# Performance work log

Hardware: AMD Instinct MI355X
Metric: run time of the kernel (lower is better)

## Reference

```python
import jax, jax.numpy as jnp
import numpy as np

EPS = 1e-7
ATTN_W_EPS = float(np.sqrt(EPS))
RESIDUAL_SCALE = 1.0


def mish(v):
    return v * jnp.tanh(jax.nn.softplus(v))


def setup_inputs() -> dict:
    key = jax.random.key(0)
    ks = jax.random.split(key, 12)
    N, E, dim, hidden = 100000, 500000, 128, 128
    x = jax.random.normal(ks[0], (N, dim), dtype=jnp.float32)
    edge_attr = jax.random.normal(ks[1], (E, dim), dtype=jnp.float32)
    head_node_index = jax.random.randint(ks[2], (E,), 0, N)
    tail_node_index = jax.random.randint(ks[3], (E,), 0, N)
    node_batch = jax.random.randint(ks[4], (N,), 0, 8)
    edge_batch = jax.random.randint(ks[5], (E,), 0, 8)
    s_in = 1.0 / np.sqrt(dim)
    s_out = 1.0 / np.sqrt(hidden)
    W_node_in = jax.random.normal(ks[6], (dim, 4 * hidden), dtype=jnp.float32) * s_in
    W_edge_in = jax.random.normal(ks[7], (dim, 3 * hidden), dtype=jnp.float32) * s_in
    node_message_bias = jnp.zeros((hidden,), dtype=jnp.float32)
    edge_message_bias = jnp.zeros((hidden,), dtype=jnp.float32)
    W_node_out = jax.random.normal(ks[8], (hidden, dim), dtype=jnp.float32) * s_out
    b_node_out = jnp.zeros((dim,), dtype=jnp.float32)
    W_edge_out = jax.random.normal(ks[9], (hidden, dim), dtype=jnp.float32) * s_out
    b_edge_out = jnp.zeros((dim,), dtype=jnp.float32)
    return {
        'x': x, 'edge_attr': edge_attr,
        'head_node_index': head_node_index, 'tail_node_index': tail_node_index,
        'node_batch': node_batch, 'edge_batch': edge_batch,
        'num_nodes': N, 'num_graphs': 8,
        'W_node_in': W_node_in, 'W_edge_in': W_edge_in,
        'node_message_bias': node_message_bias, 'edge_message_bias': edge_message_bias,
        'W_node_out': W_node_out, 'b_node_out': b_node_out,
        'W_edge_out': W_edge_out, 'b_edge_out': b_edge_out,
    }


def reference(x, edge_attr, head_node_index, tail_node_index, node_batch, edge_batch,
              num_nodes, num_graphs, W_node_in, W_edge_in,
              node_message_bias, edge_message_bias,
              W_node_out, b_node_out, W_edge_out, b_edge_out):
    hidden = node_message_bias.shape[0]
    # node input linear -> 4 chunks
    node_messages = x @ W_node_in  # [N, 4*hidden]
    node_to_self, node_to_neighbor, head_to_edge, tail_to_edge = jnp.split(node_messages, 4, axis=-1)
    node_to_edge = head_to_edge[head_node_index] + tail_to_edge[tail_node_index]  # [E, hidden]
    # edge input linear -> 3 chunks
    edge_messages = edge_attr @ W_edge_in  # [E, 3*hidden]
    edge_to_self, edge_to_tail, edge_attn_message = jnp.split(edge_messages, 3, axis=-1)
    # segment-softmax-style attention weight (max detached, per tail node)
    seg_max = jax.ops.segment_max(jax.lax.stop_gradient(edge_attn_message), tail_node_index,
                                  num_segments=num_nodes)  # [N, hidden]
    edge_attn_weight = jnp.exp(edge_attn_message - seg_max[tail_node_index]) + ATTN_W_EPS  # [E, hidden]
    # attention-weighted scatter aggregation to tail nodes
    sent = (node_to_neighbor[head_node_index] + edge_to_tail) * edge_attn_weight  # [E, hidden]
    received = jax.ops.segment_sum(sent, tail_node_index, num_segments=num_nodes)
    recv_weight = jax.ops.segment_sum(edge_attn_weight, tail_node_index, num_segments=num_nodes)
    node_received = received / (recv_weight + EPS)  # [N, hidden]
    # node output path
    x_residual = mish(node_received + node_to_self + node_message_bias) @ W_node_out + b_node_out
    x_out = x + RESIDUAL_SCALE * x_residual
    # edge output path
    e_residual = mish(node_to_edge + edge_to_self + edge_message_bias) @ W_edge_out + b_edge_out
    edge_attr_out = edge_attr + RESIDUAL_SCALE * e_residual
    return (x_out, edge_attr_out)
```

## Files before the change

kernel.cpp:

```cpp
#include <hip/hip_runtime.h>
#include <hip/hip_bf16.h>
#include <math.h>

typedef short bf16x8 __attribute__((ext_vector_type(8)));
typedef float f32x4 __attribute__((ext_vector_type(4)));
typedef unsigned int u32;
typedef unsigned short u16;

#define DIM 128
#define ATTN_EPS 3.1622776601683794e-4f
#define DIV_EPS 1e-7f
#define SCAN_BLKS 256

__device__ __forceinline__ u16 f2b(float f) {
  u32 u = __float_as_uint(f);
  return (u16)((u + 0x7FFFu + ((u >> 16) & 1u)) >> 16);
}
__device__ __forceinline__ float b2f(u16 s) { return __uint_as_float(((u32)s) << 16); }
__device__ __forceinline__ float mish_f(float v) {
  float e = __expf(fminf(v, 15.f));
  float w = 1.f + e;
  return v * (1.f - 2.f * __builtin_amdgcn_rcpf(w * w + 1.f));
}

template <int NT, int NR>
__device__ __forceinline__ void stage_f32(u16 (*dst)[136], const float* __restrict__ src,
                                          long rowbase, long nrows, int tid) {
  #pragma unroll
  for (int it = 0; it < NR * 16 / NT; ++it) {
    int i = it * NT + tid;
    int r = i >> 4, c = (i & 15) * 8;
    long gr = rowbase + r;
    bf16x8 v;
    if (gr < nrows) {
      const f32x4* p = (const f32x4*)(src + gr * (long)DIM + c);
      f32x4 a = p[0], b = p[1];
      #pragma unroll
      for (int j = 0; j < 4; ++j) { v[j] = (short)f2b(a[j]); v[j + 4] = (short)f2b(b[j]); }
    } else {
      #pragma unroll
      for (int j = 0; j < 8; ++j) v[j] = 0;
    }
    *(bf16x8*)&dst[r][c] = v;
  }
}

template <int NT, int NR>
__device__ __forceinline__ void stage_b16(u16 (*dst)[136], const u16* __restrict__ src, int tid) {
  #pragma unroll
  for (int it = 0; it < NR * 16 / NT; ++it) {
    int i = it * NT + tid;
    int r = i >> 4, c = (i & 15) * 8;
    *(bf16x8*)&dst[r][c] = *(const bf16x8*)&src[(long)r * DIM + c];
  }
}

template <int NT, int NR>
__device__ __forceinline__ void gather_nm(u16 (*dst)[136], const u16* __restrict__ nm,
    const int* __restrict__ idx, int segoff, long rowbase, long nrows, int tid) {
  #pragma unroll
  for (int it = 0; it < NR * 16 / NT; ++it) {
    int i = it * NT + tid;
    int r = i >> 4, c = (i & 15) * 8;
    long gr = rowbase + r;
    bf16x8 v;
    if (gr < nrows) {
      v = *(const bf16x8*)&nm[(long)idx[gr] * 512 + segoff + c];
    } else {
      #pragma unroll
      for (int j = 0; j < 8; ++j) v[j] = 0;
    }
    *(bf16x8*)&dst[r][c] = v;
  }
}

__device__ __forceinline__ void mm_32x64(const u16 (*As)[136], const u16 (*Bs)[136],
                                         int wr, int wc, int lane, f32x4 acc[2][4]) {
  int r0 = wr * 32 + (lane & 15);
  int cb = wc * 64 + (lane & 15);
  int koff = (lane >> 4) * 8;
  #pragma unroll
  for (int ks = 0; ks < 4; ++ks) {
    int k = ks * 32 + koff;
    bf16x8 a0 = *(const bf16x8*)&As[r0][k];
    bf16x8 a1 = *(const bf16x8*)&As[r0 + 16][k];
    #pragma unroll
    for (int ct = 0; ct < 4; ++ct) {
      bf16x8 b = *(const bf16x8*)&Bs[cb + ct * 16][k];
      acc[0][ct] = __builtin_amdgcn_mfma_f32_16x16x32_bf16(a0, b, acc[0][ct], 0, 0, 0);
      acc[1][ct] = __builtin_amdgcn_mfma_f32_16x16x32_bf16(a1, b, acc[1][ct], 0, 0, 0);
    }
  }
}

__global__ void k_prep(const float* __restrict__ Wni, const float* __restrict__ Wei,
                       const float* __restrict__ Wno, const float* __restrict__ Weo,
                       u16* __restrict__ Tni, u16* __restrict__ Tei,
                       u16* __restrict__ Tno, u16* __restrict__ Teo,
                       u32* __restrict__ deg, int N) {
  int stride = gridDim.x * blockDim.x;
  int t0 = blockIdx.x * blockDim.x + threadIdx.x;
  for (int i = t0; i < 128 * 512; i += stride) { int k = i >> 9, c = i & 511; Tni[c * 128 + k] = f2b(Wni[i]); }
  for (int i = t0; i < 128 * 384; i += stride) { int k = i / 384, c = i % 384; Tei[c * 128 + k] = f2b(Wei[i]); }
  for (int i = t0; i < 128 * 128; i += stride) { int k = i >> 7, c = i & 127; Tno[c * 128 + k] = f2b(Wno[i]); }
  for (int i = t0; i < 128 * 128; i += stride) { int k = i >> 7, c = i & 127; Teo[c * 128 + k] = f2b(Weo[i]); }
  for (int i = t0; i < N; i += stride) deg[i] = 0;
}

__global__ __launch_bounds__(512, 4) void k_node_in(const float* __restrict__ x,
    const u16* __restrict__ Tni, u16* __restrict__ nm, int N) {
  __shared__ u16 As[128][136];
  __shared__ u16 Bs[128][136];
  int tid = threadIdx.x, lane = tid & 63;
  int wid = tid >> 6, wr = wid >> 1, wc = wid & 1;
  long rowbase = (long)blockIdx.x * 128;
  stage_f32<512, 128>(As, x, rowbase, N, tid);
  stage_b16<512, 128>(Bs, Tni, tid);
  __syncthreads();
  #pragma unroll 1
  for (int chunk = 0; chunk < 4; ++chunk) {
    f32x4 acc[2][4] = {};
    mm_32x64(As, Bs, wr, wc, lane, acc);
    __syncthreads();
    if (chunk < 3) stage_b16<512, 128>(Bs, Tni + (chunk + 1) * 128 * DIM, tid);
    #pragma unroll
    for (int rt = 0; rt < 2; ++rt)
    #pragma unroll
    for (int j = 0; j < 4; ++j) {
      int lr = wr * 32 + rt * 16 + ((lane >> 4) << 2) + j;
      long r = rowbase + lr;
      if (r >= N) continue;
      #pragma unroll
      for (int ct = 0; ct < 4; ++ct) {
        int col = wc * 64 + ct * 16 + (lane & 15);
        nm[r * 512 + chunk * 128 + col] = f2b(acc[rt][ct][j]);
      }
    }
    if (chunk < 3) __syncthreads();
  }
}

__global__ __launch_bounds__(512, 4) void k_edge_in(const float* __restrict__ ea,
    const u16* __restrict__ Tei, const u16* __restrict__ Teo,
    const u16* __restrict__ nm, const int* __restrict__ head, const int* __restrict__ tail,
    const float* __restrict__ ebias, const float* __restrict__ beo,
    u32* __restrict__ em, float* __restrict__ eout, int E) {
  __shared__ u16 As[128][136];
  __shared__ u16 Bs[128][136];
  int tid = threadIdx.x, lane = tid & 63;
  int wid = tid >> 6, wr = wid >> 1, wc = wid & 1;
  long rowbase = (long)blockIdx.x * 128;
  int col0 = wc * 64 + (lane & 15);

  stage_f32<512, 128>(As, ea, rowbase, E, tid);
  stage_b16<512, 128>(Bs, Tei + 128 * DIM, tid);
  __syncthreads();
  f32x4 acc_t[2][4] = {};
  mm_32x64(As, Bs, wr, wc, lane, acc_t);
  __syncthreads();
  stage_b16<512, 128>(Bs, Tei + 256 * DIM, tid);
  __syncthreads();
  f32x4 acc_m[2][4] = {};
  mm_32x64(As, Bs, wr, wc, lane, acc_m);
  __syncthreads();
  gather_nm<512, 128>(Bs, nm, head, 128, rowbase, E, tid);
  __syncthreads();
  #pragma unroll
  for (int rt = 0; rt < 2; ++rt)
  #pragma unroll
  for (int j = 0; j < 4; ++j) {
    int lr = wr * 32 + rt * 16 + ((lane >> 4) << 2) + j;
    long r = rowbase + lr;
    if (r < E) {
      #pragma unroll
      for (int ct = 0; ct < 4; ++ct) {
        int col = col0 + ct * 16;
        float n2n = b2f(Bs[lr][col]);
        em[r * 128 + col] = (u32)f2b(n2n + acc_t[rt][ct][j])
                          | ((u32)f2b(acc_m[rt][ct][j]) << 16);
      }
    }
  }
  __syncthreads();
  stage_b16<512, 128>(Bs, Tei, tid);
  __syncthreads();
  f32x4 acc_s[2][4] = {};
  mm_32x64(As, Bs, wr, wc, lane, acc_s);
  __syncthreads();
  gather_nm<512, 128>(Bs, nm, head, 256, rowbase, E, tid);
  gather_nm<512, 128>(As, nm, tail, 384, rowbase, E, tid);
  __syncthreads();
  #pragma unroll
  for (int rt = 0; rt < 2; ++rt)
  #pragma unroll
  for (int j = 0; j < 4; ++j) {
    int lr = wr * 32 + rt * 16 + ((lane >> 4) << 2) + j;
    long r = rowbase + lr;
    #pragma unroll
    for (int ct = 0; ct < 4; ++ct) {
      int col = col0 + ct * 16;
      if (r < E) {
        float epre = acc_s[rt][ct][j] + b2f(Bs[lr][col]) + b2f(As[lr][col]) + ebias[col];
        As[lr][col] = f2b(mish_f(epre));
      } else {
        As[lr][col] = 0;
      }
    }
  }
  __syncthreads();
  stage_b16<512, 128>(Bs, Teo, tid);
  __syncthreads();
  f32x4 acc_o[2][4] = {};
  mm_32x64(As, Bs, wr, wc, lane, acc_o);
  #pragma unroll
  for (int rt = 0; rt < 2; ++rt)
  #pragma unroll
  for (int j = 0; j < 4; ++j) {
    int lr = wr * 32 + rt * 16 + ((lane >> 4) << 2) + j;
    long r = rowbase + lr;
    if (r >= E) continue;
    #pragma unroll
    for (int ct = 0; ct < 4; ++ct) {
      int col = col0 + ct * 16;
      eout[r * DIM + col] = ea[r * DIM + col] + acc_o[rt][ct][j] + beo[col];
    }
  }
}

__global__ void k_count(const int* __restrict__ tail, u32* __restrict__ deg, int E) {
  int i = blockIdx.x * blockDim.x + threadIdx.x;
  int stride = gridDim.x * blockDim.x;
  for (; i < E; i += stride) atomicAdd(&deg[tail[i]], 1u);
}
__global__ __launch_bounds__(256) void k_scan_part(const u32* __restrict__ deg,
                                                   u32* __restrict__ part, int N) {
  __shared__ u32 red[256];
  int tid = threadIdx.x, b = blockIdx.x;
  int chunk = (N + SCAN_BLKS - 1) / SCAN_BLKS;
  int lo = b * chunk, hi = min(lo + chunk, N);
  u32 s = 0;
  for (int i = lo + tid; i < hi; i += 256) s += deg[i];
  red[tid] = s; __syncthreads();
  for (int st = 128; st > 0; st >>= 1) { if (tid < st) red[tid] += red[tid + st]; __syncthreads(); }
  if (tid == 0) part[b] = red[0];
}
__global__ __launch_bounds__(256) void k_scan_mid(u32* __restrict__ part) {
  __shared__ u32 lds[256];
  int tid = threadIdx.x;
  u32 v = part[tid];
  lds[tid] = v; __syncthreads();
  for (int s = 1; s < 256; s <<= 1) {
    u32 a = (tid >= s) ? lds[tid - s] : 0; __syncthreads();
    lds[tid] += a; __syncthreads();
  }
  part[tid] = lds[tid] - v;
}
__global__ __launch_bounds__(256) void k_scan_fin(const u32* __restrict__ deg,
    const u32* __restrict__ part, u32* __restrict__ off, u32* __restrict__ cur, int N) {
  __shared__ u32 lds[256];
  int tid = threadIdx.x, b = blockIdx.x;
  int chunk = (N + SCAN_BLKS - 1) / SCAN_BLKS;
  int lo = b * chunk, hi = min(lo + chunk, N);
  u32 carry = part[b];
  for (int base = lo; base < hi; base += 256) {
    int i = base + tid;
    u32 v = (i < hi) ? deg[i] : 0;
    lds[tid] = v; __syncthreads();
    for (int s = 1; s < 256; s <<= 1) {
      u32 a = (tid >= s) ? lds[tid - s] : 0; __syncthreads();
      lds[tid] += a; __syncthreads();
    }
    u32 incl = lds[tid], total = lds[255];
    __syncthreads();
    if (i < hi) { u32 o = carry + incl - v; off[i] = o; cur[i] = o; }
    carry += total;
  }
}
__global__ void k_fill(const int* __restrict__ tail, u32* __restrict__ cur,
                       u32* __restrict__ csr, int E) {
  int i = blockIdx.x * blockDim.x + threadIdx.x;
  int stride = gridDim.x * blockDim.x;
  for (; i < E; i += stride) { u32 p = atomicAdd(&cur[tail[i]], 1u); csr[p] = (u32)i; }
}

__global__ __launch_bounds__(256, 8) void k_node_agg(const u32* __restrict__ em,
    const u16* __restrict__ nm, const u32* __restrict__ off, const u32* __restrict__ deg,
    const u32* __restrict__ csr, const float* __restrict__ nbias,
    u16* __restrict__ hbuf, int N) {
  int tid = threadIdx.x, lane = tid & 63;
  int node = blockIdx.x * 4 + (tid >> 6);
  if (node >= N) return;
  int ch = lane * 2;
  u32 o = __builtin_amdgcn_readfirstlane(off[node]);
  u32 d = __builtin_amdgcn_readfirstlane(deg[node]);
  float m0 = -INFINITY, m1 = -INFINITY;
  float s0 = 0.f, s1 = 0.f, v0 = 0.f, v1 = 0.f, sv0 = 0.f, sv1 = 0.f;
  for (u32 i = 0; i < d; i += 4) {
    uint2 b[4];
    #pragma unroll
    for (int j = 0; j < 4; ++j) {
      if (i + j < d) {
        u32 e = csr[o + i + j];
        b[j] = *(const uint2*)(em + (long)e * 128 + ch);
      } else {
        b[j].x = 0xFF800000u; b[j].y = 0xFF800000u;
      }
    }
    #pragma unroll
    for (int j = 0; j < 4; ++j) {
      float val0 = b2f((u16)(b[j].x & 0xffff)), g0 = b2f((u16)(b[j].x >> 16));
      float val1 = b2f((u16)(b[j].y & 0xffff)), g1 = b2f((u16)(b[j].y >> 16));
      float nmx0 = fmaxf(m0, g0);
      float sc0 = __expf(m0 - nmx0), pe0 = __expf(g0 - nmx0);
      s0 = s0 * sc0 + pe0; v0 = v0 * sc0 + pe0 * val0; sv0 += val0; m0 = nmx0;
      float nmx1 = fmaxf(m1, g1);
      float sc1 = __expf(m1 - nmx1), pe1 = __expf(g1 - nmx1);
      s1 = s1 * sc1 + pe1; v1 = v1 * sc1 + pe1 * val1; sv1 += val1; m1 = nmx1;
    }
  }
  float de = (float)d * ATTN_EPS;
  float r0 = (v0 + ATTN_EPS * sv0) * __builtin_amdgcn_rcpf(s0 + de + DIV_EPS);
  float r1 = (v1 + ATTN_EPS * sv1) * __builtin_amdgcn_rcpf(s1 + de + DIV_EPS);
  u32 np = *(const u32*)&nm[(long)node * 512 + ch];
  float h0 = mish_f(r0 + b2f((u16)(np & 0xffff)) + nbias[ch]);
  float h1 = mish_f(r1 + b2f((u16)(np >> 16)) + nbias[ch + 1]);
  *(u32*)&hbuf[(long)node * 128 + ch] = (u32)f2b(h0) | ((u32)f2b(h1) << 16);
}

__global__ __launch_bounds__(256) void k_node_out(const float* __restrict__ x,
    const u16* __restrict__ hbuf, const u16* __restrict__ Tno, const float* __restrict__ bno,
    float* __restrict__ xout, int N) {
  __shared__ u16 As[64][136];
  __shared__ u16 Bs[128][136];
  int tid = threadIdx.x, lane = tid & 63;
  int wid = tid >> 6, wr = wid >> 1, wc = wid & 1;
  long rowbase = (long)blockIdx.x * 64;
  stage_b16<256, 64>(As, hbuf + rowbase * DIM, tid);
  stage_b16<256, 128>(Bs, Tno, tid);
  __syncthreads();
  f32x4 acc[2][4] = {};
  mm_32x64(As, Bs, wr, wc, lane, acc);
  #pragma unroll
  for (int rt = 0; rt < 2; ++rt)
  #pragma unroll
  for (int j = 0; j < 4; ++j) {
    int lr = wr * 32 + rt * 16 + ((lane >> 4) << 2) + j;
    long r = rowbase + lr;
    if (r >= N) continue;
    #pragma unroll
    for (int ct = 0; ct < 4; ++ct) {
      int col = wc * 64 + ct * 16 + (lane & 15);
      xout[r * DIM + col] = x[r * DIM + col] + acc[rt][ct][j] + bno[col];
    }
  }
}

extern "C" void kernel_launch(void* const* d_in, const int* in_sizes, int n_in,
                              void* d_out, int out_size, void* d_ws, size_t ws_size,
                              hipStream_t stream) {
  const float* x     = (const float*)d_in[0];
  const float* ea    = (const float*)d_in[1];
  const int*   head  = (const int*)d_in[2];
  const int*   tail  = (const int*)d_in[3];
  const float* Wni   = (const float*)d_in[8];
  const float* Wei   = (const float*)d_in[9];
  const float* nbias = (const float*)d_in[10];
  const float* ebias = (const float*)d_in[11];
  const float* Wno   = (const float*)d_in[12];
  const float* bno   = (const float*)d_in[13];
  const float* Weo   = (const float*)d_in[14];
  const float* beo   = (const float*)d_in[15];
  const int N = in_sizes[0] / DIM;
  const int E = in_sizes[1] / DIM;
  const int NB64 = (N + 63) / 64;
  const int NB128 = (N + 127) / 128;
  const int EB = (E + 127) / 128;
  const int NPAD = NB64 * 64;

  char* ws = (char*)d_ws;
  u16*   nm   = (u16*)ws; ws += (size_t)N * 512 * 2;
  u32*   em   = (u32*)ws; ws += (size_t)E * 128 * 4;
  u16*   hbuf = (u16*)ws; ws += (size_t)NPAD * 128 * 2;
  u32*   deg  = (u32*)ws; ws += (size_t)N * 4;
  u32*   off  = (u32*)ws; ws += (size_t)N * 4;
  u32*   cur  = (u32*)ws; ws += (size_t)N * 4;
  u32*   part = (u32*)ws; ws += (size_t)SCAN_BLKS * 4;
  u32*   csr  = (u32*)ws; ws += (size_t)E * 4;
  u16* Tni = (u16*)ws; ws += 512 * DIM * 2;
  u16* Tei = (u16*)ws; ws += 384 * DIM * 2;
  u16* Tno = (u16*)ws; ws += DIM * DIM * 2;
  u16* Teo = (u16*)ws; ws += DIM * DIM * 2;

  float* xout = (float*)d_out;
  float* eout = xout + (size_t)N * DIM;

  k_prep<<<256, 256, 0, stream>>>(Wni, Wei, Wno, Weo, Tni, Tei, Tno, Teo, deg, N);
  k_count<<<512, 256, 0, stream>>>(tail, deg, E);
  k_scan_part<<<SCAN_BLKS, 256, 0, stream>>>(deg, part, N);
  k_scan_mid<<<1, 256, 0, stream>>>(part);
  k_scan_fin<<<SCAN_BLKS, 256, 0, stream>>>(deg, part, off, cur, N);
  k_fill<<<512, 256, 0, stream>>>(tail, cur, csr, E);
  k_node_in<<<NB128, 512, 0, stream>>>(x, Tni, nm, N);
  k_edge_in<<<EB, 512, 0, stream>>>(ea, Tei, Teo, nm, head, tail, ebias, beo, em, eout, E);
  k_node_agg<<<(N + 3) / 4, 256, 0, stream>>>(em, nm, off, deg, csr, nbias, hbuf, N);
  k_node_out<<<NB64, 256, 0, stream>>>(x, hbuf, Tno, bno, xout, N);
}
```

Before: 557.2 us.

## Fuse node aggregation with node output GEMM via LDS-staged hidden tile

Merges the attention aggregation kernel and the node output matmul into a single kernel. Each 512-thread block aggregates 64 nodes (8 per wave), writes the mish-activated hidden rows into shared memory, then runs the 64x128 output GEMM directly from LDS. This removes the hbuf round trip through global memory and one kernel launch. The trade-offs are a serial loop of 8 nodes per wave, which reduces latency hiding on the irregular gathers, and extra LDS per block, which may lower occupancy.

```diff
diff --git a/kernel.cpp b/kernel.cpp
--- a/kernel.cpp
+++ b/kernel.cpp
@@ -86,6 +86,25 @@
     bf16x8 a1 = *(const bf16x8*)&As[r0 + 16][k];
     #pragma unroll
     for (int ct = 0; ct < 4; ++ct) {
+      bf16x8 b = *(const bf16x8*)&Bs[cb + ct * 16][k];
+      acc[0][ct] = __builtin_amdgcn_mfma_f32_16x16x32_bf16(a0, b, acc[0][ct], 0, 0, 0);
+      acc[1][ct] = __builtin_amdgcn_mfma_f32_16x16x32_bf16(a1, b, acc[1][ct], 0, 0, 0);
+    }
+  }
+}
+
+__device__ __forceinline__ void mm_32x32(const u16 (*As)[136], const u16 (*Bs)[136],
+                                         int wr, int wc, int lane, f32x4 acc[2][2]) {
+  int r0 = wr * 32 + (lane & 15);
+  int cb = wc * 32 + (lane & 15);
+  int koff = (lane >> 4) * 8;
+  #pragma unroll
+  for (int ks = 0; ks < 4; ++ks) {
+    int k = ks * 32 + koff;
+    bf16x8 a0 = *(const bf16x8*)&As[r0][k];
+    bf16x8 a1 = *(const bf16x8*)&As[r0 + 16][k];
+    #pragma unroll
+    for (int ct = 0; ct < 2; ++ct) {
       bf16x8 b = *(const bf16x8*)&Bs[cb + ct * 16][k];
       acc[0][ct] = __builtin_amdgcn_mfma_f32_16x16x32_bf16(a0, b, acc[0][ct], 0, 0, 0);
       acc[1][ct] = __builtin_amdgcn_mfma_f32_16x16x32_bf16(a1, b, acc[1][ct], 0, 0, 0);
@@ -283,63 +302,65 @@
   for (; i < E; i += stride) { u32 p = atomicAdd(&cur[tail[i]], 1u); csr[p] = (u32)i; }
 }
 
-__global__ __launch_bounds__(256, 8) void k_node_agg(const u32* __restrict__ em,
+__global__ __launch_bounds__(512, 6) void k_agg_out(const u32* __restrict__ em,
     const u16* __restrict__ nm, const u32* __restrict__ off, const u32* __restrict__ deg,
-    const u32* __restrict__ csr, const float* __restrict__ nbias,
-    u16* __restrict__ hbuf, int N) {
-  int tid = threadIdx.x, lane = tid & 63;
-  int node = blockIdx.x * 4 + (tid >> 6);
-  if (node >= N) return;
+    const u32* __restrict__ csr, const float* __restrict__ nbias, const float* __restrict__ x,
+    const u16* __restrict__ Tno, const float* __restrict__ bno,
+    float* __restrict__ xout, int N) {
+  __shared__ u16 Hs[64][136];
+  __shared__ u16 Bs[128][136];
+  int tid = threadIdx.x, lane = tid & 63, wid = tid >> 6;
+  long rowbase = (long)blockIdx.x * 64;
   int ch = lane * 2;
-  u32 o = __builtin_amdgcn_readfirstlane(off[node]);
-  u32 d = __builtin_amdgcn_readfirstlane(deg[node]);
-  float m0 = -INFINITY, m1 = -INFINITY;
-  float s0 = 0.f, s1 = 0.f, v0 = 0.f, v1 = 0.f, sv0 = 0.f, sv1 = 0.f;
-  for (u32 i = 0; i < d; i += 4) {
-    uint2 b[4];
-    #pragma unroll
-    for (int j = 0; j < 4; ++j) {
-      if (i + j < d) {
-        u32 e = csr[o + i + j];
-        b[j] = *(const uint2*)(em + (long)e * 128 + ch);
-      } else {
-        b[j].x = 0xFF800000u; b[j].y = 0xFF800000u;
+  stage_b16<512, 128>(Bs, Tno, tid);
+  float nb0 = nbias[ch], nb1 = nbias[ch + 1];
+  #pragma unroll 1
+  for (int s = 0; s < 8; ++s) {
+    int lr = wid * 8 + s;
+    long node = rowbase + lr;
+    u32 hpack = 0;
+    if (node < N) {
+      u32 o = __builtin_amdgcn_readfirstlane(off[node]);
+      u32 d = __builtin_amdgcn_readfirstlane(deg[node]);
+      float m0 = -INFINITY, m1 = -INFINITY;
+      float s0 = 0.f, s1 = 0.f, v0 = 0.f, v1 = 0.f, sv0 = 0.f, sv1 = 0.f;
+      for (u32 i = 0; i < d; i += 4) {
+        uint2 b[4];
+        #pragma unroll
+        for (int j = 0; j < 4; ++j) {
+          if (i + j < d) {
+            u32 e = csr[o + i + j];
+            b[j] = *(const uint2*)(em + (long)e * 128 + ch);
+          } else {
+            b[j].x = 0xFF800000u; b[j].y = 0xFF800000u;
+          }
+        }
+        #pragma unroll
+        for (int j = 0; j < 4; ++j) {
+          float val0 = b2f((u16)(b[j].x & 0xffff)), g0 = b2f((u16)(b[j].x >> 16));
+          float val1 = b2f((u16)(b[j].y & 0xffff)), g1 = b2f((u16)(b[j].y >> 16));
+          float nmx0 = fmaxf(m0, g0);
+          float sc0 = __expf(m0 - nmx0), pe0 = __expf(g0 - nmx0);
+          s0 = s0 * sc0 + pe0; v0 = v0 * sc0 + pe0 * val0; sv0 += val0; m0 = nmx0;
+          float nmx1 = fmaxf(m1, g1);
+          float sc1 = __expf(m1 - nmx1), pe1 = __expf(g1 - nmx1);
+          s1 = s1 * sc1 + pe1; v1 = v1 * sc1 + pe1 * val1; sv1 += val1; m1 = nmx1;
+        }
       }
-    }
-    #pragma unroll
-    for (int j = 0; j < 4; ++j) {
-      float val0 = b2f((u16)(b[j].x & 0xffff)), g0 = b2f((u16)(b[j].x >> 16));
-      float val1 = b2f((u16)(b[j].y & 0xffff)), g1 = b2f((u16)(b[j].y >> 16));
-      float nmx0 = fmaxf(m0, g0);
-      float sc0 = __expf(m0 - nmx0), pe0 = __expf(g0 - nmx0);
-      s0 = s0 * sc0 + pe0; v0 = v0 * sc0 + pe0 * val0; sv0 += val0; m0 = nmx0;
-      float nmx1 = fmaxf(m1, g1);
-      float sc1 = __expf(m1 - nmx1), pe1 = __expf(g1 - nmx1);
-      s1 = s1 * sc1 + pe1; v1 = v1 * sc1 + pe1 * val1; sv1 += val1; m1 = nmx1;
-    }
-  }
-  float de = (float)d * ATTN_EPS;
-  float r0 = (v0 + ATTN_EPS * sv0) * __builtin_amdgcn_rcpf(s0 + de + DIV_EPS);
-  float r1 = (v1 + ATTN_EPS * sv1) * __builtin_amdgcn_rcpf(s1 + de + DIV_EPS);
-  u32 np = *(const u32*)&nm[(long)node * 512 + ch];
-  float h0 = mish_f(r0 + b2f((u16)(np & 0xffff)) + nbias[ch]);
-  float h1 = mish_f(r1 + b2f((u16)(np >> 16)) + nbias[ch + 1]);
-  *(u32*)&hbuf[(long)node * 128 + ch] = (u32)f2b(h0) | ((u32)f2b(h1) << 16);
-}
-
-__global__ __launch_bounds__(256) void k_node_out(const float* __restrict__ x,
-    const u16* __restrict__ hbuf, const u16* __restrict__ Tno, const float* __restrict__ bno,
-    float* __restrict__ xout, int N) {
-  __shared__ u16 As[64][136];
-  __shared__ u16 Bs[128][136];
-  int tid = threadIdx.x, lane = tid & 63;
-  int wid = tid >> 6, wr = wid >> 1, wc = wid & 1;
-  long rowbase = (long)blockIdx.x * 64;
-  stage_b16<256, 64>(As, hbuf + rowbase * DIM, tid);
-  stage_b16<256, 128>(Bs, Tno, tid);
-  __syncthreads();
-  f32x4 acc[2][4] = {};
-  mm_32x64(As, Bs, wr, wc, lane, acc);
+      float de = (float)d * ATTN_EPS;
+      float r0 = (v0 + ATTN_EPS * sv0) * __builtin_amdgcn_rcpf(s0 + de + DIV_EPS);
+      float r1 = (v1 + ATTN_EPS * sv1) * __builtin_amdgcn_rcpf(s1 + de + DIV_EPS);
+      u32 np = *(const u32*)&nm[node * 512 + ch];
+      float h0 = mish_f(r0 + b2f((u16)(np & 0xffff)) + nb0);
+      float h1 = mish_f(r1 + b2f((u16)(np >> 16)) + nb1);
+      hpack = (u32)f2b(h0) | ((u32)f2b(h1) << 16);
+    }
+    *(u32*)&Hs[lr][ch] = hpack;
+  }
+  __syncthreads();
+  int wr = wid >> 2, wc = wid & 3;
+  f32x4 acc[2][2] = {};
+  mm_32x32(Hs, Bs, wr, wc, lane, acc);
   #pragma unroll
   for (int rt = 0; rt < 2; ++rt)
   #pragma unroll
@@ -348,8 +369,8 @@
     long r = rowbase + lr;
     if (r >= N) continue;
     #pragma unroll
-    for (int ct = 0; ct < 4; ++ct) {
-      int col = wc * 64 + ct * 16 + (lane & 15);
+    for (int ct = 0; ct < 2; ++ct) {
+      int col = wc * 32 + ct * 16 + (lane & 15);
       xout[r * DIM + col] = x[r * DIM + col] + acc[rt][ct][j] + bno[col];
     }
   }
@@ -375,12 +396,10 @@
   const int NB64 = (N + 63) / 64;
   const int NB128 = (N + 127) / 128;
   const int EB = (E + 127) / 128;
-  const int NPAD = NB64 * 64;
 
   char* ws = (char*)d_ws;
   u16*   nm   = (u16*)ws; ws += (size_t)N * 512 * 2;
   u32*   em   = (u32*)ws; ws += (size_t)E * 128 * 4;
-  u16*   hbuf = (u16*)ws; ws += (size_t)NPAD * 128 * 2;
   u32*   deg  = (u32*)ws; ws += (size_t)N * 4;
   u32*   off  = (u32*)ws; ws += (size_t)N * 4;
   u32*   cur  = (u32*)ws; ws += (size_t)N * 4;
@@ -402,6 +421,5 @@
   k_fill<<<512, 256, 0, stream>>>(tail, cur, csr, E);
   k_node_in<<<NB128, 512, 0, stream>>>(x, Tni, nm, N);
   k_edge_in<<<EB, 512, 0, stream>>>(ea, Tei, Teo, nm, head, tail, ebias, beo, em, eout, E);
-  k_node_agg<<<(N + 3) / 4, 256, 0, stream>>>(em, nm, off, deg, csr, nbias, hbuf, N);
-  k_node_out<<<NB64, 256, 0, stream>>>(x, hbuf, Tno, bno, xout, N);
-}
+  k_agg_out<<<NB64, 512, 0, stream>>>(em, nm, off, deg, csr, nbias, x, Tno, bno, xout, N);
+}
```

Result: slower. 571.2 us (+2.5%).
